# Kernel optimization log

Measured on AMD Instinct MI355X. Metric: run time of the kernel, lower is better.

Reference implementation:

```python
import jax, jax.numpy as jnp
import numpy as np

GROUPS = 32
EPS = 1e-5
NHEAD = 8


def group_norm(x, gamma, beta):
    # x: [B, C, T]
    B, C, T = x.shape
    xg = x.reshape(B, GROUPS, C // GROUPS, T)
    mean = xg.mean(axis=(2, 3), keepdims=True)
    var = xg.var(axis=(2, 3), keepdims=True)
    xg = (xg - mean) * jax.lax.rsqrt(var + EPS)
    x = xg.reshape(B, C, T)
    return x * gamma[None, :, None] + beta[None, :, None]


def conv1x1(x, w, b):
    # x: [B, C_in, T], w: [C_out, C_in], b: [C_out]
    return jnp.einsum('oc,bct->bot', w, x) + b[None, :, None]


def setup_inputs() -> dict:
    key = jax.random.key(0)
    ks = jax.random.split(key, 4)
    B, C, T = 8, 512, 2048
    x = jax.random.normal(ks[0], (B, C, T), dtype=jnp.float32)
    w_qkv = jax.random.normal(ks[1], (3 * C, C), dtype=jnp.float32) * (1.0 / np.sqrt(C))
    b_qkv = jnp.zeros((3 * C,), dtype=jnp.float32)
    w_proj = jax.random.normal(ks[2], (C, C), dtype=jnp.float32) * (1.0 / np.sqrt(C))
    b_proj = jnp.zeros((C,), dtype=jnp.float32)
    return {
        'x': x,
        'gn1_gamma': jnp.ones((C,), jnp.float32), 'gn1_beta': jnp.zeros((C,), jnp.float32),
        'w_qkv': w_qkv, 'b_qkv': b_qkv,
        'gn2_gamma': jnp.ones((C,), jnp.float32), 'gn2_beta': jnp.zeros((C,), jnp.float32),
        'w_proj': w_proj, 'b_proj': b_proj,
    }


def qkv_attention(qkv):
    # qkv: [B, 3*H*ch, T] laid out as H blocks of (q ch, k ch, v ch)
    B, width, T = qkv.shape
    ch = width // (3 * NHEAD)
    qkv = qkv.reshape(B, NHEAD, 3 * ch, T)
    q, k, v = qkv[:, :, :ch], qkv[:, :, ch:2 * ch], qkv[:, :, 2 * ch:]
    scale = 1.0 / np.sqrt(np.sqrt(ch)).astype(np.float32)
    # scores: [B, H, T(q), T(k)]
    w = jnp.einsum('bhct,bhcs->bhts', q * scale, k * scale)
    w = jax.nn.softmax(w, axis=-1)  # max-subtract softmax, same math
    a = jnp.einsum('bhts,bhcs->bhct', w, v)
    return a.reshape(B, NHEAD * ch, T)


def reference(x, gn1_gamma, gn1_beta, w_qkv, b_qkv, gn2_gamma, gn2_beta, w_proj, b_proj):
    # x: [B, C, T]
    qkv = conv1x1(group_norm(x, gn1_gamma, gn1_beta), w_qkv, b_qkv)  # [B, 3C, T]
    h = qkv_attention(qkv)                                            # [B, C, T]
    h = conv1x1(group_norm(h, gn2_gamma, gn2_beta), w_proj, b_proj)   # [B, C, T]
    return x + h
```

## Files before the change

### kernel.cpp

```cpp
#include <hip/hip_runtime.h>

typedef unsigned short u16;
typedef unsigned int   u32;
typedef __attribute__((ext_vector_type(8))) short short8;
typedef __attribute__((ext_vector_type(4))) float floatx4;

__device__ inline u16 f2bf(float x) {
  union { float f; unsigned u; } v; v.f = x;
  unsigned r = v.u + 0x7FFFu + ((v.u >> 16) & 1u);
  return (u16)(r >> 16);
}
__device__ inline float bf2f(short s) {
  union { u32 u; float f; } v; v.u = ((u32)(u16)s) << 16; return v.f;
}
__device__ inline short8 ld8(const u16* p) {
  return *reinterpret_cast<const short8*>(p);
}
__device__ inline void async_ld16(const u16* g, u16* l) {
  unsigned loff = (unsigned)(unsigned long long)(void*)l;
  __builtin_amdgcn_global_load_lds(reinterpret_cast<const unsigned*>(g),
      reinterpret_cast<__attribute__((address_space(3))) unsigned*>(loff), 16, 0, 0);
}

__global__ __launch_bounds__(256) void cast_both(const float* __restrict__ s1,
                                                 u16* __restrict__ d1,
                                                 const float* __restrict__ s2,
                                                 u16* __restrict__ d2) {
  const float* src; u16* dst; int i;
  if (blockIdx.x < 768) { src = s1; dst = d1; i = blockIdx.x * 256 + threadIdx.x; }
  else                  { src = s2; dst = d2; i = (blockIdx.x - 768) * 256 + threadIdx.x; }
  float4 v = reinterpret_cast<const float4*>(src)[i];
  union { u16 u[4]; float2 f; } w;
  w.u[0] = f2bf(v.x); w.u[1] = f2bf(v.y); w.u[2] = f2bf(v.z); w.u[3] = f2bf(v.w);
  reinterpret_cast<float2*>(dst)[i] = w.f;
}

__global__ __launch_bounds__(1024) void gn_ct(const float* __restrict__ x,
                                              const float* __restrict__ gamma,
                                              const float* __restrict__ beta,
                                              u16* __restrict__ xn) {
  int b = blockIdx.x >> 5, g = blockIdx.x & 31;
  const float* base = x + ((long)b * 512 + g * 16) * 2048;
  float s = 0.f, ss = 0.f;
  for (int i = threadIdx.x; i < 8192; i += 1024) {
    float4 v = reinterpret_cast<const float4*>(base)[i];
    s  += v.x + v.y + v.z + v.w;
    ss += v.x * v.x + v.y * v.y + v.z * v.z + v.w * v.w;
  }
  #pragma unroll
  for (int d = 1; d < 64; d <<= 1) { s += __shfl_xor(s, d); ss += __shfl_xor(ss, d); }
  __shared__ float red[32];
  int wave = threadIdx.x >> 6, lane = threadIdx.x & 63;
  if (lane == 0) { red[wave] = s; red[wave + 16] = ss; }
  __syncthreads();
  s = 0.f; ss = 0.f;
  #pragma unroll
  for (int w = 0; w < 16; w++) { s += red[w]; ss += red[w + 16]; }
  float mean = s * (1.f / 32768.f);
  float var  = ss * (1.f / 32768.f) - mean * mean;
  float rstd = rsqrtf(var + 1e-5f);
  float ga[16], be[16];
  #pragma unroll
  for (int c = 0; c < 16; c++) {
    float gm = gamma[g * 16 + c];
    ga[c] = gm * rstd;
    be[c] = beta[g * 16 + c] - mean * rstd * gm;
  }
  u16* ob = xn + (long)b * 2048 * 512 + g * 16;
  for (int t = threadIdx.x; t < 2048; t += 1024) {
    union { u16 u[8]; float4 f; } w0, w1;
    #pragma unroll
    for (int c = 0; c < 8; c++)  w0.u[c]     = f2bf(base[c * 2048 + t] * ga[c] + be[c]);
    #pragma unroll
    for (int c = 8; c < 16; c++) w1.u[c - 8] = f2bf(base[c * 2048 + t] * ga[c] + be[c]);
    u16* dst = ob + (long)t * 512;
    *reinterpret_cast<float4*>(dst)     = w0.f;
    *reinterpret_cast<float4*>(dst + 8) = w1.f;
  }
}

__global__ __launch_bounds__(1024) void gn_tc(const u16* __restrict__ a,
                                              const float* __restrict__ gamma,
                                              const float* __restrict__ beta,
                                              u16* __restrict__ hn) {
  int b = blockIdx.x >> 5, g = blockIdx.x & 31;
  const u16* base = a + (long)b * 2048 * 512 + g * 16;
  float s = 0.f, ss = 0.f;
  for (int t = threadIdx.x; t < 2048; t += 1024) {
    const u16* p = base + (long)t * 512;
    short8 v0 = ld8(p), v1 = ld8(p + 8);
    #pragma unroll
    for (int j = 0; j < 8; j++) {
      float f0 = bf2f(v0[j]), f1 = bf2f(v1[j]);
      s += f0 + f1; ss += f0 * f0 + f1 * f1;
    }
  }
  #pragma unroll
  for (int d = 1; d < 64; d <<= 1) { s += __shfl_xor(s, d); ss += __shfl_xor(ss, d); }
  __shared__ float red[32];
  int wave = threadIdx.x >> 6, lane = threadIdx.x & 63;
  if (lane == 0) { red[wave] = s; red[wave + 16] = ss; }
  __syncthreads();
  s = 0.f; ss = 0.f;
  #pragma unroll
  for (int w = 0; w < 16; w++) { s += red[w]; ss += red[w + 16]; }
  float mean = s * (1.f / 32768.f);
  float var  = ss * (1.f / 32768.f) - mean * mean;
  float rstd = rsqrtf(var + 1e-5f);
  float ga[16], be[16];
  #pragma unroll
  for (int c = 0; c < 16; c++) {
    float gm = gamma[g * 16 + c];
    ga[c] = gm * rstd;
    be[c] = beta[g * 16 + c] - mean * rstd * gm;
  }
  u16* ob = hn + (long)b * 2048 * 512 + g * 16;
  for (int t = threadIdx.x; t < 2048; t += 1024) {
    const u16* p = base + (long)t * 512;
    short8 v0 = ld8(p), v1 = ld8(p + 8);
    union { u16 u[8]; float4 f; } w0, w1;
    #pragma unroll
    for (int c = 0; c < 8; c++)  w0.u[c] = f2bf(bf2f(v0[c]) * ga[c] + be[c]);
    #pragma unroll
    for (int c = 0; c < 8; c++)  w1.u[c] = f2bf(bf2f(v1[c]) * ga[c + 8] + be[c + 8]);
    u16* dst = ob + (long)t * 512;
    *reinterpret_cast<float4*>(dst)     = w0.f;
    *reinterpret_cast<float4*>(dst + 8) = w1.f;
  }
}

template<int QKV>
__global__ __launch_bounds__(256) void gemm_tn(
    const u16* __restrict__ A, long abst,
    const u16* __restrict__ Bt, long bbst,
    const float* __restrict__ bias,
    const float* __restrict__ resid, long rbst,
    void* __restrict__ outp, long obst,
    u16* __restrict__ vtp, int K) {
  __shared__ __align__(16) u16 As[128 * 32];
  __shared__ __align__(16) u16 Bs[128 * 32];
  const int tid = threadIdx.x;
  const int m0 = blockIdx.y * 128, n0 = blockIdx.x * 128;
  const int N = gridDim.x * 128;
  const long bz = blockIdx.z;
  const u16* Ab = A + bz * abst + (long)m0 * K;
  const u16* Bb = Bt + bz * bbst + (long)n0 * K;
  const int lane = tid & 63, wave = tid >> 6;
  const int wm = (wave & 1) * 64, wn = (wave >> 1) * 64;
  const int l15 = lane & 15, quad = lane >> 4;
  const u16* ag[2]; const u16* bg[2];
  const int ldso = wave * 512;
  #pragma unroll
  for (int half = 0; half < 2; half++) {
    int r = half * 64 + (tid >> 2);
    ag[half] = Ab + (long)r * K + (tid & 3) * 8;
    bg[half] = Bb + (long)r * K + (tid & 3) * 8;
  }

  floatx4 acc[4][4];
  #pragma unroll
  for (int i = 0; i < 4; i++)
    #pragma unroll
    for (int j = 0; j < 4; j++) acc[i][j] = (floatx4){0.f, 0.f, 0.f, 0.f};

  for (int k0 = 0; k0 < K; k0 += 32) {
    __syncthreads();
    #pragma unroll
    for (int half = 0; half < 2; half++) {
      async_ld16(ag[half] + k0, &As[half * 2048 + ldso]);
      async_ld16(bg[half] + k0, &Bs[half * 2048 + ldso]);
    }
    __syncthreads();
    short8 af[4], bfr[4];
    #pragma unroll
    for (int i = 0; i < 4; i++) af[i]  = ld8(&As[(wm + i * 16 + l15) * 32 + quad * 8]);
    #pragma unroll
    for (int i = 0; i < 4; i++) bfr[i] = ld8(&Bs[(wn + i * 16 + l15) * 32 + quad * 8]);
    #pragma unroll
    for (int mi = 0; mi < 4; mi++)
      #pragma unroll
      for (int ni = 0; ni < 4; ni++)
        acc[mi][ni] = __builtin_amdgcn_mfma_f32_16x16x32_bf16(af[mi], bfr[ni], acc[mi][ni], 0, 0, 0);
  }

  if (QKV) {
    u16* D  = (u16*)outp + bz * obst;
    u16* VT = vtp + bz * (8L * 64 * 2048);
    #pragma unroll
    for (int ni = 0; ni < 4; ni++) {
      int nb = n0 + wn + ni * 16;
      int region = (nb >> 6) % 3;
      int n = nb + l15;
      float bn = bias[n];
      if (region == 2) {
        int hh = n / 192, c = (n % 192) - 128;
        u16* vrow = VT + ((long)hh * 64 + c) * 2048 + m0 + wm;
        #pragma unroll
        for (int mi = 0; mi < 4; mi++) {
          union { u16 u[4]; float2 f; } pk;
          #pragma unroll
          for (int r = 0; r < 4; r++) pk.u[r] = f2bf(acc[mi][ni][r] + bn);
          *reinterpret_cast<float2*>(vrow + mi * 16 + quad * 4) = pk.f;
        }
      } else {
        float sc = (region == 0) ? 0.180336880f : 1.f;
        #pragma unroll
        for (int mi = 0; mi < 4; mi++)
          #pragma unroll
          for (int r = 0; r < 4; r++) {
            int m = m0 + wm + mi * 16 + quad * 4 + r;
            D[(long)m * 1536 + n] = f2bf((acc[mi][ni][r] + bn) * sc);
          }
      }
    }
  } else {
    float* D = (float*)outp + bz * obst;
    const float* R = resid + bz * rbst;
    #pragma unroll
    for (int mi = 0; mi < 4; mi++)
      #pragma unroll
      for (int r = 0; r < 4; r++) {
        int m = m0 + wm + mi * 16 + quad * 4 + r;
        float bm = bias[m];
        #pragma unroll
        for (int ni = 0; ni < 4; ni++) {
          int n = n0 + wn + ni * 16 + l15;
          long idx = (long)m * N + n;
          D[idx] = acc[mi][ni][r] + bm + R[idx];
        }
      }
  }
}

__global__ __launch_bounds__(256, 2) void attn(const u16* __restrict__ qkv,
                                               const u16* __restrict__ vt,
                                               u16* __restrict__ aout) {
  __shared__ __align__(16) u16 Ps[256 * 64];
  __shared__ __align__(16) u16 Ks[2][64 * 64];
  __shared__ __align__(16) u16 Vs[2][64 * 64];
  const int tid = threadIdx.x, lane = tid & 63, wave = tid >> 6;
  const int l15 = lane & 15, quad = lane >> 4;
  const int sw = l15 & 7;
  const int b = blockIdx.y >> 3, h = blockIdx.y & 7;
  const int t0 = blockIdx.x * 256;
  const u16* qbase = qkv + (long)b * 2048 * 1536 + h * 192;
  const u16* vbase = vt + (long)(b * 8 + h) * 64 * 2048;

  short8 qf[4][2];
  #pragma unroll
  for (int tqi = 0; tqi < 4; tqi++)
    #pragma unroll
    for (int ks = 0; ks < 2; ks++)
      qf[tqi][ks] = ld8(qbase + (long)(t0 + wave * 64 + tqi * 16 + l15) * 1536 + ks * 32 + quad * 8);

  short8 ones;
  #pragma unroll
  for (int j = 0; j < 8; j++) ones[j] = (short)0x3F80;

  const u16* kg[2]; const u16* vg[2]; int ldso[2];
  #pragma unroll
  for (int half = 0; half < 2; half++) {
    int p = half * 256 + wave * 64 + lane;
    int row = p >> 3, c = (p & 7) ^ (row & 7);
    kg[half] = qbase + (long)row * 1536 + 64 + c * 8;
    vg[half] = vbase + (long)row * 2048 + c * 8;
    ldso[half] = (half * 256 + wave * 64) * 8;
  }
  #pragma unroll
  for (int half = 0; half < 2; half++) {
    async_ld16(kg[half], &Ks[0][ldso[half]]);
    async_ld16(vg[half], &Vs[0][ldso[half]]);
  }

  floatx4 accO[4][4];
  floatx4 lacc[4];
  #pragma unroll
  for (int ci = 0; ci < 4; ci++)
    #pragma unroll
    for (int tqi = 0; tqi < 4; tqi++) accO[ci][tqi] = (floatx4){0.f, 0.f, 0.f, 0.f};
  #pragma unroll
  for (int tqi = 0; tqi < 4; tqi++) lacc[tqi] = (floatx4){0.f, 0.f, 0.f, 0.f};

  for (int it = 0; it < 32; it++) {
    const u16* kb = Ks[it & 1];
    const u16* vb = Vs[it & 1];
    __syncthreads();
    if (it < 31) {
      int s1 = (it + 1) * 64;
      u16* kn = Ks[(it & 1) ^ 1];
      u16* vn = Vs[(it & 1) ^ 1];
      #pragma unroll
      for (int half = 0; half < 2; half++) {
        async_ld16(kg[half] + (long)s1 * 1536, &kn[ldso[half]]);
        async_ld16(vg[half] + s1,              &vn[ldso[half]]);
      }
    }

    floatx4 sacc[4][4];
    #pragma unroll
    for (int i = 0; i < 4; i++)
      #pragma unroll
      for (int j = 0; j < 4; j++) sacc[i][j] = (floatx4){0.f, 0.f, 0.f, 0.f};
    #pragma unroll
    for (int ks = 0; ks < 2; ks++) {
      short8 kf[4];
      #pragma unroll
      for (int tki = 0; tki < 4; tki++)
        kf[tki] = ld8(&kb[((tki * 16 + l15) << 6) + (((ks * 4 + quad) ^ sw) << 3)]);
      #pragma unroll
      for (int tki = 0; tki < 4; tki++)
        #pragma unroll
        for (int tqi = 0; tqi < 4; tqi++)
          sacc[tki][tqi] = __builtin_amdgcn_mfma_f32_16x16x32_bf16(kf[tki], qf[tqi][ks], sacc[tki][tqi], 0, 0, 0);
    }

    #pragma unroll
    for (int tqi = 0; tqi < 4; tqi++) {
      int prow = (wave * 64 + tqi * 16 + l15) << 6;
      #pragma unroll
      for (int tki = 0; tki < 4; tki++) {
        float p0 = __builtin_amdgcn_exp2f(sacc[tki][tqi][0]);
        float p1 = __builtin_amdgcn_exp2f(sacc[tki][tqi][1]);
        float p2 = __builtin_amdgcn_exp2f(sacc[tki][tqi][2]);
        float p3 = __builtin_amdgcn_exp2f(sacc[tki][tqi][3]);
        union { u32 u[2]; float2 f; } pk;
        pk.u[0] = __builtin_amdgcn_perm(__float_as_uint(p1), __float_as_uint(p0), 0x07060302);
        pk.u[1] = __builtin_amdgcn_perm(__float_as_uint(p3), __float_as_uint(p2), 0x07060302);
        int c16 = tki * 2 + (quad >> 1);
        *reinterpret_cast<float2*>(
            &Ps[prow + ((c16 ^ sw) << 3) + ((quad & 1) << 2)]) = pk.f;
      }
    }

    #pragma unroll
    for (int ks = 0; ks < 2; ks++) {
      short8 vf[4], pf[4];
      #pragma unroll
      for (int ci = 0; ci < 4; ci++)
        vf[ci] = ld8(&vb[((ci * 16 + l15) << 6) + (((ks * 4 + quad) ^ sw) << 3)]);
      #pragma unroll
      for (int tqi = 0; tqi < 4; tqi++)
        pf[tqi] = ld8(&Ps[((wave * 64 + tqi * 16 + l15) << 6) + (((ks * 4 + quad) ^ sw) << 3)]);
      #pragma unroll
      for (int tqi = 0; tqi < 4; tqi++)
        lacc[tqi] = __builtin_amdgcn_mfma_f32_16x16x32_bf16(ones, pf[tqi], lacc[tqi], 0, 0, 0);
      #pragma unroll
      for (int ci = 0; ci < 4; ci++)
        #pragma unroll
        for (int tqi = 0; tqi < 4; tqi++)
          accO[ci][tqi] = __builtin_amdgcn_mfma_f32_16x16x32_bf16(vf[ci], pf[tqi], accO[ci][tqi], 0, 0, 0);
    }
  }

  u16* ob = aout + ((long)b * 2048 + t0 + wave * 64) * 512 + h * 64;
  #pragma unroll
  for (int tqi = 0; tqi < 4; tqi++) {
    float invl = 1.f / lacc[tqi][0];
    #pragma unroll
    for (int ci = 0; ci < 4; ci++) {
      union { u16 u[4]; float2 f; } pk;
      #pragma unroll
      for (int r = 0; r < 4; r++) pk.u[r] = f2bf(accO[ci][tqi][r] * invl);
      *reinterpret_cast<float2*>(ob + (long)(tqi * 16 + l15) * 512 + ci * 16 + quad * 4) = pk.f;
    }
  }
}

extern "C" void kernel_launch(void* const* d_in, const int* in_sizes, int n_in,
                              void* d_out, int out_size, void* d_ws, size_t ws_size,
                              hipStream_t stream) {
  const float* x   = (const float*)d_in[0];
  const float* g1  = (const float*)d_in[1];
  const float* be1 = (const float*)d_in[2];
  const float* wq  = (const float*)d_in[3];
  const float* bq  = (const float*)d_in[4];
  const float* g2  = (const float*)d_in[5];
  const float* be2 = (const float*)d_in[6];
  const float* wp  = (const float*)d_in[7];
  const float* bp  = (const float*)d_in[8];

  char* ws = (char*)d_ws;
  u16*   xn   = (u16*)ws;
  u16*   a    = (u16*)ws;
  u16*   qkvb = (u16*)(ws + 33554432);
  u16*   hn   = (u16*)(ws + 83886080);
  u16*   vtb  = hn;
  u16*   wqb  = (u16*)(ws + 100663296);
  u16*   wpb  = (u16*)(ws + 102236160);

  cast_both<<<1024, 256, 0, stream>>>(wq, wqb, wp, wpb);
  gn_ct<<<256, 1024, 0, stream>>>(x, g1, be1, xn);
  gemm_tn<1><<<dim3(12, 16, 8), 256, 0, stream>>>(
      xn, (long)2048 * 512, wqb, 0, bq, nullptr, 0, qkvb, (long)2048 * 1536, vtb, 512);
  attn<<<dim3(8, 64), 256, 0, stream>>>(qkvb, vtb, a);
  gn_tc<<<256, 1024, 0, stream>>>(a, g2, be2, hn);
  gemm_tn<0><<<dim3(16, 4, 8), 256, 0, stream>>>(
      wpb, 0, hn, (long)2048 * 512, bp, x, (long)512 * 2048, d_out, (long)512 * 2048, nullptr, 512);
}
```

Baseline: 284.0 us.

## Double-buffer GEMM LDS tiles and shrink attention P buffer to raise occupancy

The GEMM now double-buffers its A/B LDS tiles. It prefetches the next k-slice with async global-to-LDS loads while computing the current one, which removes one barrier per iteration. The attention kernel splits its P staging buffer into per-wave 64x32 halves that are written and consumed one ks chunk at a time, cutting LDS use so launch bounds can target 3 blocks per CU. The costs are higher GEMM LDS usage and possible extra register pressure in attention from the tighter occupancy target. The GEMM prefetch relies on barrier ordering so the buffer being loaded is never one still being read.

```diff
diff --git a/kernel.cpp b/kernel.cpp
--- a/kernel.cpp
+++ b/kernel.cpp
@@ -137,8 +137,8 @@
     const float* __restrict__ resid, long rbst,
     void* __restrict__ outp, long obst,
     u16* __restrict__ vtp, int K) {
-  __shared__ __align__(16) u16 As[128 * 32];
-  __shared__ __align__(16) u16 Bs[128 * 32];
+  __shared__ __align__(16) u16 As[2][128 * 32];
+  __shared__ __align__(16) u16 Bs[2][128 * 32];
   const int tid = threadIdx.x;
   const int m0 = blockIdx.y * 128, n0 = blockIdx.x * 128;
   const int N = gridDim.x * 128;
@@ -163,19 +163,28 @@
     #pragma unroll
     for (int j = 0; j < 4; j++) acc[i][j] = (floatx4){0.f, 0.f, 0.f, 0.f};
 
-  for (int k0 = 0; k0 < K; k0 += 32) {
+  #pragma unroll
+  for (int half = 0; half < 2; half++) {
+    async_ld16(ag[half], &As[0][half * 2048 + ldso]);
+    async_ld16(bg[half], &Bs[0][half * 2048 + ldso]);
+  }
+  const int nk = K >> 5;
+  for (int ki = 0; ki < nk; ki++) {
     __syncthreads();
-    #pragma unroll
-    for (int half = 0; half < 2; half++) {
-      async_ld16(ag[half] + k0, &As[half * 2048 + ldso]);
-      async_ld16(bg[half] + k0, &Bs[half * 2048 + ldso]);
-    }
-    __syncthreads();
+    if (ki + 1 < nk) {
+      int k1 = (ki + 1) << 5, bsel = (ki + 1) & 1;
+      #pragma unroll
+      for (int half = 0; half < 2; half++) {
+        async_ld16(ag[half] + k1, &As[bsel][half * 2048 + ldso]);
+        async_ld16(bg[half] + k1, &Bs[bsel][half * 2048 + ldso]);
+      }
+    }
+    const u16* as = As[ki & 1]; const u16* bs = Bs[ki & 1];
     short8 af[4], bfr[4];
     #pragma unroll
-    for (int i = 0; i < 4; i++) af[i]  = ld8(&As[(wm + i * 16 + l15) * 32 + quad * 8]);
-    #pragma unroll
-    for (int i = 0; i < 4; i++) bfr[i] = ld8(&Bs[(wn + i * 16 + l15) * 32 + quad * 8]);
+    for (int i = 0; i < 4; i++) af[i]  = ld8(&as[(wm + i * 16 + l15) * 32 + quad * 8]);
+    #pragma unroll
+    for (int i = 0; i < 4; i++) bfr[i] = ld8(&bs[(wn + i * 16 + l15) * 32 + quad * 8]);
     #pragma unroll
     for (int mi = 0; mi < 4; mi++)
       #pragma unroll
@@ -232,19 +241,21 @@
   }
 }
 
-__global__ __launch_bounds__(256, 2) void attn(const u16* __restrict__ qkv,
+__global__ __launch_bounds__(256, 3) void attn(const u16* __restrict__ qkv,
                                                const u16* __restrict__ vt,
                                                u16* __restrict__ aout) {
-  __shared__ __align__(16) u16 Ps[256 * 64];
+  __shared__ __align__(16) u16 Ps[4][64 * 32];
   __shared__ __align__(16) u16 Ks[2][64 * 64];
   __shared__ __align__(16) u16 Vs[2][64 * 64];
   const int tid = threadIdx.x, lane = tid & 63, wave = tid >> 6;
   const int l15 = lane & 15, quad = lane >> 4;
   const int sw = l15 & 7;
+  const int sw2 = l15 & 3;
   const int b = blockIdx.y >> 3, h = blockIdx.y & 7;
   const int t0 = blockIdx.x * 256;
   const u16* qbase = qkv + (long)b * 2048 * 1536 + h * 192;
   const u16* vbase = vt + (long)(b * 8 + h) * 64 * 2048;
+  u16* PsW = &Ps[wave][0];
 
   short8 qf[4][2];
   #pragma unroll
@@ -315,32 +326,32 @@
     }
 
     #pragma unroll
-    for (int tqi = 0; tqi < 4; tqi++) {
-      int prow = (wave * 64 + tqi * 16 + l15) << 6;
-      #pragma unroll
-      for (int tki = 0; tki < 4; tki++) {
-        float p0 = __builtin_amdgcn_exp2f(sacc[tki][tqi][0]);
-        float p1 = __builtin_amdgcn_exp2f(sacc[tki][tqi][1]);
-        float p2 = __builtin_amdgcn_exp2f(sacc[tki][tqi][2]);
-        float p3 = __builtin_amdgcn_exp2f(sacc[tki][tqi][3]);
-        union { u32 u[2]; float2 f; } pk;
-        pk.u[0] = __builtin_amdgcn_perm(__float_as_uint(p1), __float_as_uint(p0), 0x07060302);
-        pk.u[1] = __builtin_amdgcn_perm(__float_as_uint(p3), __float_as_uint(p2), 0x07060302);
-        int c16 = tki * 2 + (quad >> 1);
-        *reinterpret_cast<float2*>(
-            &Ps[prow + ((c16 ^ sw) << 3) + ((quad & 1) << 2)]) = pk.f;
+    for (int ks = 0; ks < 2; ks++) {
+      #pragma unroll
+      for (int tqi = 0; tqi < 4; tqi++) {
+        int prow = (tqi * 16 + l15) << 5;
+        #pragma unroll
+        for (int th = 0; th < 2; th++) {
+          int tki = ks * 2 + th;
+          float p0 = __builtin_amdgcn_exp2f(sacc[tki][tqi][0]);
+          float p1 = __builtin_amdgcn_exp2f(sacc[tki][tqi][1]);
+          float p2 = __builtin_amdgcn_exp2f(sacc[tki][tqi][2]);
+          float p3 = __builtin_amdgcn_exp2f(sacc[tki][tqi][3]);
+          union { u32 u[2]; float2 f; } pk;
+          pk.u[0] = __builtin_amdgcn_perm(__float_as_uint(p1), __float_as_uint(p0), 0x07060302);
+          pk.u[1] = __builtin_amdgcn_perm(__float_as_uint(p3), __float_as_uint(p2), 0x07060302);
+          int c4 = th * 2 + (quad >> 1);
+          *reinterpret_cast<float2*>(
+              &PsW[prow + (((c4 ^ sw2) << 3) | ((quad & 1) << 2))]) = pk.f;
+        }
       }
-    }
-
-    #pragma unroll
-    for (int ks = 0; ks < 2; ks++) {
       short8 vf[4], pf[4];
       #pragma unroll
       for (int ci = 0; ci < 4; ci++)
         vf[ci] = ld8(&vb[((ci * 16 + l15) << 6) + (((ks * 4 + quad) ^ sw) << 3)]);
       #pragma unroll
       for (int tqi = 0; tqi < 4; tqi++)
-        pf[tqi] = ld8(&Ps[((wave * 64 + tqi * 16 + l15) << 6) + (((ks * 4 + quad) ^ sw) << 3)]);
+        pf[tqi] = ld8(&PsW[((tqi * 16 + l15) << 5) + ((quad ^ sw2) << 3)]);
       #pragma unroll
       for (int tqi = 0; tqi < 4; tqi++)
         lacc[tqi] = __builtin_amdgcn_mfma_f32_16x16x32_bf16(ones, pf[tqi], lacc[tqi], 0, 0, 0);
```

After: 480.6 us. 1.69x slower.
